# Optimization experiments

Measured on AMD Instinct MI355X. Metric: run time of the kernel, lower is better.

## Reference

```python
import jax, jax.numpy as jnp
import numpy as np

K_HOPS = 10
ALPHA = 0.1


def setup_inputs() -> dict:
    key = jax.random.key(0)
    ks = jax.random.split(key, 12)
    B, H, N, IC, F, C = 4096, 5, 30, 256, 512, 4
    real = jax.random.normal(ks[0], (B, N, IC), jnp.float32)
    imag = jax.random.normal(ks[1], (B, N, IC), jnp.float32)
    graph = jax.random.normal(ks[2], (B, H, N, N), jnp.float32)
    def lin(k, fan_in, shape):
        s = 1.0 / np.sqrt(fan_in)
        return jax.random.uniform(k, shape, jnp.float32, -s, s)
    W1 = lin(ks[3], IC, (IC, F)); b1 = lin(ks[4], IC, (F,))
    W2 = lin(ks[5], F, (F, F));  b2 = lin(ks[6], F, (F,))
    Wl = lin(ks[7], F, (F, 1));  bl = lin(ks[8], F, (1,))
    Wc = lin(ks[9], N, (C, N));  bc = lin(ks[10], N, (C,))
    return {"real": real, "imag": imag, "graph": graph,
            "W1": W1, "b1": b1, "W2": W2, "b2": b2,
            "Wl": Wl, "bl": bl, "Wc": Wc, "bc": bc}


def _appnp(S, x):
    # x_{k+1} = alpha * x0 + (1 - alpha) * S @ x_k, K iterations
    x0 = x
    def step(h, _):
        h = ALPHA * x0 + (1.0 - ALPHA) * jnp.einsum('bij,bjf->bif', S, h)
        return h, None
    h, _ = jax.lax.scan(step, x, None, length=K_HOPS)
    return h


def _prop_matrix(graph):
    # adj = mean over frequency dim; edges = nonzero entries (weights discarded
    # by the original code), self loops added, symmetric gcn_norm with
    # degree = column sums; source->target flow => operator is transposed.
    adj = jnp.mean(graph, axis=1)                      # [B,N,N]
    M = (adj != 0).astype(graph.dtype)
    N = M.shape[-1]
    Mt = M + jnp.eye(N, dtype=graph.dtype)             # add self loops
    deg = jnp.sum(Mt, axis=-2)                         # in-degree (col sums) [B,N]
    dinv = jax.lax.rsqrt(deg)
    S = dinv[:, :, None] * jnp.swapaxes(Mt, -1, -2) * dinv[:, None, :]
    return S


def reference(real, imag, graph, W1, b1, W2, b2, Wl, bl, Wc, bc):
    S = _prop_matrix(graph)
    # layer 1: linear -> relu -> APPNP(K=10)
    x = jax.nn.relu(jnp.einsum('bni,if->bnf', real, W1) + b1)
    x = _appnp(S, x)
    # layer 2: linear -> relu -> APPNP(K=10)
    x = jax.nn.relu(jnp.einsum('bnf,fg->bng', x, W2) + b2)
    x = _appnp(S, x)
    # readout: per-node linear to scalar, relu, then Conv1d(30->C, k=1)
    x = jax.nn.relu(jnp.einsum('bnf,fo->bno', x, Wl)[..., 0] + bl[0])  # [B,N]
    out = jnp.einsum('bn,cn->bc', x, Wc) + bc                          # [B,C]
    return out
```

## Files before the change

### kernel.cpp

```cpp
#include <hip/hip_runtime.h>
#include <hip/hip_bf16.h>

typedef _Float16 f16;
typedef _Float16 f16x8 __attribute__((ext_vector_type(8)));
typedef _Float16 f16x4 __attribute__((ext_vector_type(4)));
typedef float f32x4 __attribute__((ext_vector_type(4)));

#define P_OFF   0
#define W1T_OFF 14745600
#define W2T_OFF 15007744

__global__ __launch_bounds__(256) void k_prep(const float* __restrict__ W1,
                                              const float* __restrict__ W2,
                                              f16* __restrict__ w1t,
                                              f16* __restrict__ w2t) {
    long id = (long)blockIdx.x * 256 + threadIdx.x;
    if (id < 131072) {
        int f = (int)(id >> 8), k = (int)(id & 255);
        w1t[id] = (f16)W1[k * 512 + f];
    } else {
        long i = id - 131072;
        int f = (int)(i >> 9), k = (int)(i & 511);
        w2t[i] = (f16)W2[k * 512 + f];
    }
}

__global__ __launch_bounds__(256) void k_prop(const float* __restrict__ graph,
                                              float* __restrict__ P) {
    __shared__ float MtS[4][990];
    __shared__ float dinvS[4][32];
    __shared__ f16 qhS[4][1024];
    __shared__ f16 qlS[4][1024];

    const int wv = threadIdx.x >> 6, lane = threadIdx.x & 63;
    const int lr = lane & 15, gq = lane >> 4;
    const long b = (long)blockIdx.x * 4 + wv;
    const float* g = graph + b * 4500;
    float* Mt = MtS[wv];
    float* dinv = dinvS[wv];
    f16* qh = qhS[wv];
    f16* ql = qlS[wv];

    for (int rep = 0; rep < 15; ++rep) {
        int e = rep * 64 + lane;
        if (e < 900) {
            float s = g[e] + g[900 + e] + g[1800 + e] + g[2700 + e] + g[3600 + e];
            int r = e / 30, c = e - r * 30;
            Mt[r * 33 + c] = ((s != 0.f) ? 1.f : 0.f) + ((r == c) ? 1.f : 0.f);
        }
    }
    __syncthreads();
    if (lane < 30) {
        float d = 0.f;
        #pragma unroll
        for (int r = 0; r < 30; ++r) d += Mt[r * 33 + lane];
        dinv[lane] = 1.0f / sqrtf(d);
    }
    __syncthreads();

    auto Sval = [&](int i, int j) -> float {
        if (i >= 30 || j >= 30) return 0.f;
        return dinv[i] * Mt[j * 33 + i] * dinv[j];
    };

    f16x8 sh[2], sl[2];
    #pragma unroll
    for (int mi = 0; mi < 2; ++mi)
        #pragma unroll
        for (int jj = 0; jj < 8; ++jj) {
            float v = Sval(mi * 16 + lr, gq * 8 + jj);
            f16 h = (f16)v;
            sh[mi][jj] = h;
            sl[mi][jj] = (f16)(v - (float)h);
        }

    f32x4 qd[2][2], racc[2][2];
    #pragma unroll
    for (int mi = 0; mi < 2; ++mi)
        #pragma unroll
        for (int ni = 0; ni < 2; ++ni)
            #pragma unroll
            for (int r = 0; r < 4; ++r) {
                int row = mi * 16 + gq * 4 + r, col = ni * 16 + lr;
                qd[mi][ni][r] = Sval(row, col);
                racc[mi][ni][r] = (row == col) ? 0.1f : 0.f;
            }

    float c = 0.1f;
    for (int k = 1; k <= 9; ++k) {
        c *= 0.9f;
        #pragma unroll
        for (int mi = 0; mi < 2; ++mi)
            #pragma unroll
            for (int ni = 0; ni < 2; ++ni) {
                racc[mi][ni] += c * qd[mi][ni];
                f16x4 hh, ll;
                #pragma unroll
                for (int r = 0; r < 4; ++r) {
                    float v = qd[mi][ni][r];
                    f16 h = (f16)v;
                    hh[r] = h;
                    ll[r] = (f16)(v - (float)h);
                }
                const int col = ni * 16 + lr, rowb = mi * 16 + gq * 4;
                *reinterpret_cast<f16x4*>(qh + col * 32 + rowb) = hh;
                *reinterpret_cast<f16x4*>(ql + col * 32 + rowb) = ll;
            }
        __syncthreads();
        f16x8 bh[2], bl[2];
        #pragma unroll
        for (int ni = 0; ni < 2; ++ni) {
            const int col = ni * 16 + lr;
            bh[ni] = *reinterpret_cast<const f16x8*>(qh + col * 32 + gq * 8);
            bl[ni] = *reinterpret_cast<const f16x8*>(ql + col * 32 + gq * 8);
        }
        #pragma unroll
        for (int mi = 0; mi < 2; ++mi)
            #pragma unroll
            for (int ni = 0; ni < 2; ++ni) {
                f32x4 d = {0.f, 0.f, 0.f, 0.f};
                d = __builtin_amdgcn_mfma_f32_16x16x32_f16(sh[mi], bh[ni], d, 0, 0, 0);
                d = __builtin_amdgcn_mfma_f32_16x16x32_f16(sh[mi], bl[ni], d, 0, 0, 0);
                d = __builtin_amdgcn_mfma_f32_16x16x32_f16(sl[mi], bh[ni], d, 0, 0, 0);
                qd[mi][ni] = d;
            }
        __syncthreads();
    }
    const float cf = 0.3486784401f;
    #pragma unroll
    for (int mi = 0; mi < 2; ++mi)
        #pragma unroll
        for (int ni = 0; ni < 2; ++ni)
            #pragma unroll
            for (int r = 0; r < 4; ++r) {
                int row = mi * 16 + gq * 4 + r, col = ni * 16 + lr;
                if (row < 30 && col < 30)
                    P[b * 900 + row * 30 + col] = racc[mi][ni][r] + cf * qd[mi][ni][r];
            }
}

#define SMEM_BYTES 152576
#define PF_OFF   131072
#define B1L_OFF  141312
#define B2L_OFF  143360
#define WLL_OFF  145408
#define RED_OFF  147456
#define VL_OFF   151552
#define ZL_OFF   152064

__global__ __launch_bounds__(512, 2) void k_main(
    const float* __restrict__ real, const f16* __restrict__ w1t,
    const f16* __restrict__ w2t, const float* __restrict__ b1,
    const float* __restrict__ b2, const float* __restrict__ wl,
    const float* __restrict__ bl, const float* __restrict__ wc,
    const float* __restrict__ bc, const float* __restrict__ Pws,
    float* __restrict__ out) {
    extern __shared__ char smem[];
    char*  buf = smem;
    f16*   Pf  = (f16*)(smem + PF_OFF);
    float* b1l = (float*)(smem + B1L_OFF);
    float* b2l = (float*)(smem + B2L_OFF);
    float* wll = (float*)(smem + WLL_OFF);
    float* red = (float*)(smem + RED_OFF);
    float* vl  = (float*)(smem + VL_OFF);
    float* zl  = (float*)(smem + ZL_OFF);

    const int tid  = threadIdx.x;
    const int lane = tid & 63;
    const int wv   = tid >> 6;
    const int gq   = lane >> 4;
    const int lr   = lane & 15;
    const int blk  = blockIdx.x;
    const long r0  = (long)blk * 120;

    const float* rbase = real + r0 * 256;
    #pragma unroll
    for (int i = 0; i < 16; ++i) {
        const int row = wv + 8 * i;
        const int rr  = row & 31;
        if (rr < 30) {
            const float* gp = rbase + ((long)((row >> 5) * 30 + rr)) * 256
                              + ((lane ^ wv) << 2);
            __builtin_amdgcn_global_load_lds(
                (const __attribute__((address_space(1))) unsigned int*)gp,
                (__attribute__((address_space(3))) unsigned int*)(buf + row * 1024),
                16, 0, 0);
        }
    }
    {
        const int i   = tid >> 6;
        const int row = ((i >> 1) << 5) + 30 + (i & 1);
        f32x4 z = {0.f, 0.f, 0.f, 0.f};
        *reinterpret_cast<f32x4*>(buf + row * 1024 + (tid & 63) * 16) = z;
    }
    #pragma unroll
    for (int s = 0; s < 8; ++s) {
        int e = tid + s * 512;
        int bb = e >> 10, idx = e & 1023, n = idx >> 5, kk = idx & 31;
        float p = (n < 30 && kk < 30)
            ? Pws[((long)blk * 4 + bb) * 900 + n * 30 + kk] : 0.f;
        Pf[bb * 1280 + n * 40 + kk] = (f16)p;
    }
    b1l[tid] = b1[tid];
    b2l[tid] = b2[tid];
    wll[tid] = wl[tid];

    f32x4 acc[4][8];
    #pragma unroll
    for (int a = 0; a < 4; ++a)
        #pragma unroll
        for (int b = 0; b < 8; ++b) { f32x4 z = {0.f,0.f,0.f,0.f}; acc[a][b] = z; }
    __syncthreads();

    const f16* w1p = w1t + (wv * 64 + lr) * 256;
    #pragma unroll
    for (int kc = 0; kc < 8; ++kc) {
        f16x8 wa[4];
        #pragma unroll
        for (int mi = 0; mi < 4; ++mi)
            wa[mi] = *reinterpret_cast<const f16x8*>(w1p + mi * 4096 + kc * 32 + gq * 8);
        f16x8 bf[8];
        #pragma unroll
        for (int ni = 0; ni < 8; ++ni) {
            const int row = ni * 16 + lr;
            const int cb  = kc * 128 + gq * 32;
            f32x4 a0 = *reinterpret_cast<const f32x4*>(
                buf + row * 1024 + (cb ^ ((row & 7) << 4)));
            f32x4 a1 = *reinterpret_cast<const f32x4*>(
                buf + row * 1024 + ((cb + 16) ^ ((row & 7) << 4)));
            f16x8 h;
            h[0]=(f16)a0[0]; h[1]=(f16)a0[1]; h[2]=(f16)a0[2]; h[3]=(f16)a0[3];
            h[4]=(f16)a1[0]; h[5]=(f16)a1[1]; h[6]=(f16)a1[2]; h[7]=(f16)a1[3];
            bf[ni] = h;
        }
        __builtin_amdgcn_s_setprio(1);
        #pragma unroll
        for (int mi = 0; mi < 4; ++mi)
            #pragma unroll
            for (int ni = 0; ni < 8; ++ni)
                acc[mi][ni] = __builtin_amdgcn_mfma_f32_16x16x32_f16(wa[mi], bf[ni], acc[mi][ni], 0, 0, 0);
        __builtin_amdgcn_s_setprio(0);
    }
    __syncthreads();

    #pragma unroll
    for (int mi = 0; mi < 4; ++mi) {
        const int featb = wv * 64 + mi * 16 + gq * 4;
        float b1v[4];
        #pragma unroll
        for (int j = 0; j < 4; ++j) b1v[j] = b1l[featb + j];
        #pragma unroll
        for (int ni = 0; ni < 8; ++ni) {
            const int node = ni * 16 + lr;
            f16x4 h;
            #pragma unroll
            for (int j = 0; j < 4; ++j)
                h[j] = (f16)fmaxf(acc[mi][ni][j] + b1v[j], 0.f);
            *reinterpret_cast<f16x4*>(
                buf + node * 1024 + ((featb * 2) ^ ((node & 15) << 4))) = h;
        }
    }
    #pragma unroll
    for (int a = 0; a < 4; ++a)
        #pragma unroll
        for (int b = 0; b < 8; ++b) { f32x4 z = {0.f,0.f,0.f,0.f}; acc[a][b] = z; }
    __syncthreads();

    const f16* w2p = w2t + (wv * 64 + lr) * 512;
    f16x8 bfA[4], bfB[4];
    #pragma unroll
    for (int ni = 0; ni < 4; ++ni)
        bfA[ni] = *reinterpret_cast<const f16x8*>(w2p + ni * 8192 + gq * 8);
    #pragma unroll
    for (int ni = 0; ni < 4; ++ni)
        bfB[ni] = *reinterpret_cast<const f16x8*>(w2p + ni * 8192 + 32 + gq * 8);
    #pragma unroll
    for (int kc2 = 0; kc2 < 8; ++kc2) {
        {
            const int kc = 2 * kc2;
            f16x8 af[8];
            #pragma unroll
            for (int mi = 0; mi < 8; ++mi) {
                const int row = mi * 16 + lr;
                af[mi] = *reinterpret_cast<const f16x8*>(
                    buf + row * 1024 + (((kc * 32 + gq * 8) * 2) ^ ((row & 15) << 4)));
            }
            __builtin_amdgcn_s_setprio(1);
            #pragma unroll
            for (int mi = 0; mi < 8; ++mi)
                #pragma unroll
                for (int ni = 0; ni < 4; ++ni)
                    acc[ni][mi] = __builtin_amdgcn_mfma_f32_16x16x32_f16(af[mi], bfA[ni], acc[ni][mi], 0, 0, 0);
            __builtin_amdgcn_s_setprio(0);
            if (kc + 2 < 16)
                #pragma unroll
                for (int ni = 0; ni < 4; ++ni)
                    bfA[ni] = *reinterpret_cast<const f16x8*>(w2p + ni * 8192 + (kc + 2) * 32 + gq * 8);
        }
        {
            const int kc = 2 * kc2 + 1;
            f16x8 af[8];
            #pragma unroll
            for (int mi = 0; mi < 8; ++mi) {
                const int row = mi * 16 + lr;
                af[mi] = *reinterpret_cast<const f16x8*>(
                    buf + row * 1024 + (((kc * 32 + gq * 8) * 2) ^ ((row & 15) << 4)));
            }
            __builtin_amdgcn_s_setprio(1);
            #pragma unroll
            for (int mi = 0; mi < 8; ++mi)
                #pragma unroll
                for (int ni = 0; ni < 4; ++ni)
                    acc[ni][mi] = __builtin_amdgcn_mfma_f32_16x16x32_f16(af[mi], bfB[ni], acc[ni][mi], 0, 0, 0);
            __builtin_amdgcn_s_setprio(0);
            if (kc + 2 < 16)
                #pragma unroll
                for (int ni = 0; ni < 4; ++ni)
                    bfB[ni] = *reinterpret_cast<const f16x8*>(w2p + ni * 8192 + (kc + 2) * 32 + gq * 8);
        }
    }
    __syncthreads();

    #pragma unroll
    for (int mi = 0; mi < 8; ++mi)
        #pragma unroll
        for (int ni = 0; ni < 4; ++ni) {
            const int feat  = wv * 64 + ni * 16 + lr;
            const int node0 = mi * 16 + gq * 4;
            f16x4 h;
            #pragma unroll
            for (int j = 0; j < 4; ++j) h[j] = (f16)acc[ni][mi][j];
            *reinterpret_cast<f16x4*>(
                buf + feat * 256 + ((node0 * 2) ^ ((feat & 15) << 4))) = h;
        }
    __syncthreads();

    {
        f16x8 pb[4][2];
        #pragma unroll
        for (int bb = 0; bb < 4; ++bb)
            #pragma unroll
            for (int ni = 0; ni < 2; ++ni)
                pb[bb][ni] = *reinterpret_cast<const f16x8*>(
                    Pf + bb * 1280 + (ni * 16 + lr) * 40 + gq * 8);
        float vacc[4][2];
        #pragma unroll
        for (int bb = 0; bb < 4; ++bb)
            #pragma unroll
            for (int ni = 0; ni < 2; ++ni) vacc[bb][ni] = 0.f;
        #pragma unroll
        for (int mi = 0; mi < 4; ++mi) {
            const int featb = wv * 64 + mi * 16;
            float b2v[4], wlv[4];
            #pragma unroll
            for (int j = 0; j < 4; ++j) {
                b2v[j] = b2l[featb + gq * 4 + j];
                wlv[j] = wll[featb + gq * 4 + j];
            }
            f16x8 au[4];
            #pragma unroll
            for (int bb = 0; bb < 4; ++bb) {
                const int feat = featb + lr;
                au[bb] = *reinterpret_cast<const f16x8*>(
                    buf + feat * 256 + ((bb * 64 + gq * 16) ^ ((feat & 15) << 4)));
            }
            #pragma unroll
            for (int bb = 0; bb < 4; ++bb)
                #pragma unroll
                for (int ni = 0; ni < 2; ++ni) {
                    f32x4 d = {0.f,0.f,0.f,0.f};
                    d = __builtin_amdgcn_mfma_f32_16x16x32_f16(au[bb], pb[bb][ni], d, 0, 0, 0);
                    #pragma unroll
                    for (int j = 0; j < 4; ++j) {
                        float y = fmaxf(d[j] + b2v[j], 0.f);
                        vacc[bb][ni] = fmaf(y, wlv[j], vacc[bb][ni]);
                    }
                }
        }
        #pragma unroll
        for (int bb = 0; bb < 4; ++bb)
            #pragma unroll
            for (int ni = 0; ni < 2; ++ni) {
                float v = vacc[bb][ni];
                v += __shfl_xor(v, 16);
                v += __shfl_xor(v, 32);
                if (lane < 16) red[wv * 128 + bb * 32 + ni * 16 + lr] = v;
            }
    }
    __syncthreads();
    if (tid < 128) {
        float s = 0.f;
        #pragma unroll
        for (int w = 0; w < 8; ++w) s += red[w * 128 + tid];
        vl[tid] = s;
    }
    __syncthreads();
    if (tid < 120) {
        const int bb = tid / 30, n = tid - bb * 30;
        const float* Pr = Pws + ((long)blk * 4 + bb) * 900 + n * 30;
        float z = bl[0];
        #pragma unroll
        for (int j = 0; j < 30; ++j) z = fmaf(Pr[j], vl[bb * 32 + j], z);
        zl[tid] = fmaxf(z, 0.f);
    }
    __syncthreads();
    if (tid < 16) {
        const int bb = tid >> 2, cc = tid & 3;
        float o = bc[cc];
        #pragma unroll
        for (int n = 0; n < 30; ++n) o = fmaf(zl[bb * 30 + n], wc[cc * 30 + n], o);
        out[((long)blk * 4 + bb) * 4 + cc] = o;
    }
}

extern "C" void kernel_launch(void* const* d_in, const int* in_sizes, int n_in,
                              void* d_out, int out_size, void* d_ws, size_t ws_size,
                              hipStream_t stream) {
    const float* real  = (const float*)d_in[0];
    const float* graph = (const float*)d_in[2];
    const float* W1    = (const float*)d_in[3];
    const float* b1    = (const float*)d_in[4];
    const float* W2    = (const float*)d_in[5];
    const float* b2    = (const float*)d_in[6];
    const float* Wl    = (const float*)d_in[7];
    const float* bl    = (const float*)d_in[8];
    const float* Wc    = (const float*)d_in[9];
    const float* bc    = (const float*)d_in[10];
    float* out = (float*)d_out;
    char*  ws  = (char*)d_ws;

    float* Pws = (float*)(ws + P_OFF);
    f16*   w1t = (f16*)(ws + W1T_OFF);
    f16*   w2t = (f16*)(ws + W2T_OFF);

    k_prep<<<1536, 256, 0, stream>>>(W1, W2, w1t, w2t);
    k_prop<<<1024, 256, 0, stream>>>(graph, Pws);
    (void)hipFuncSetAttribute((const void*)k_main,
                              hipFuncAttributeMaxDynamicSharedMemorySize, SMEM_BYTES);
    k_main<<<1024, 512, SMEM_BYTES, stream>>>(real, w1t, w2t, b1, b2, Wl, bl, Wc, bc,
                                              Pws, out);
}
```

Baseline: 184.3 us.

## Double k_main block to 1024 threads with 2D wave tiling and f16 staging

k_main now runs 16 waves per block, split into 8 feature groups by 2 node halves, so each wave holds a 4x4 MFMA accumulator tile instead of 4x8. The input rows are loaded with plain vector loads, converted to f16 and stored swizzled into LDS, replacing the async global-to-LDS fp32 copy and the per-iteration conversion. The first GEMM also gains double-buffered weight prefetch. The aim is more waves for latency hiding and lower register pressure, at the cost of an extra LDS region for the 16-wave reduction and a synchronous load phase.

```diff
diff --git a/kernel.cpp b/kernel.cpp
--- a/kernel.cpp
+++ b/kernel.cpp
@@ -139,16 +139,16 @@
             }
 }
 
-#define SMEM_BYTES 152576
+#define SMEM_BYTES 156672
 #define PF_OFF   131072
 #define B1L_OFF  141312
 #define B2L_OFF  143360
 #define WLL_OFF  145408
 #define RED_OFF  147456
-#define VL_OFF   151552
-#define ZL_OFF   152064
-
-__global__ __launch_bounds__(512, 2) void k_main(
+#define VL_OFF   155648
+#define ZL_OFF   156160
+
+__global__ __launch_bounds__(1024, 4) void k_main(
     const float* __restrict__ real, const f16* __restrict__ w1t,
     const f16* __restrict__ w2t, const float* __restrict__ b1,
     const float* __restrict__ b2, const float* __restrict__ wl,
@@ -168,90 +168,104 @@
     const int tid  = threadIdx.x;
     const int lane = tid & 63;
     const int wv   = tid >> 6;
+    const int wf   = wv & 7;
+    const int wn   = wv >> 3;
     const int gq   = lane >> 4;
     const int lr   = lane & 15;
     const int blk  = blockIdx.x;
     const long r0  = (long)blk * 120;
 
-    const float* rbase = real + r0 * 256;
-    #pragma unroll
-    for (int i = 0; i < 16; ++i) {
-        const int row = wv + 8 * i;
-        const int rr  = row & 31;
-        if (rr < 30) {
-            const float* gp = rbase + ((long)((row >> 5) * 30 + rr)) * 256
-                              + ((lane ^ wv) << 2);
-            __builtin_amdgcn_global_load_lds(
-                (const __attribute__((address_space(1))) unsigned int*)gp,
-                (__attribute__((address_space(3))) unsigned int*)(buf + row * 1024),
-                16, 0, 0);
-        }
-    }
     {
-        const int i   = tid >> 6;
-        const int row = ((i >> 1) << 5) + 30 + (i & 1);
-        f32x4 z = {0.f, 0.f, 0.f, 0.f};
-        *reinterpret_cast<f32x4*>(buf + row * 1024 + (tid & 63) * 16) = z;
-    }
-    #pragma unroll
-    for (int s = 0; s < 8; ++s) {
-        int e = tid + s * 512;
+        const int srow = tid >> 3;
+        const int seg  = tid & 7;
+        const int rr   = srow & 31;
+        const bool valid = rr < 30;
+        const float* p = real + (r0 + (long)(srow >> 5) * 30 + rr) * 256 + seg * 32;
+        #pragma unroll
+        for (int q = 0; q < 4; ++q) {
+            f32x4 v0 = {0.f,0.f,0.f,0.f}, v1 = {0.f,0.f,0.f,0.f};
+            if (valid) {
+                v0 = *reinterpret_cast<const f32x4*>(p + q * 8);
+                v1 = *reinterpret_cast<const f32x4*>(p + q * 8 + 4);
+            }
+            f16x8 h;
+            h[0]=(f16)v0[0]; h[1]=(f16)v0[1]; h[2]=(f16)v0[2]; h[3]=(f16)v0[3];
+            h[4]=(f16)v1[0]; h[5]=(f16)v1[1]; h[6]=(f16)v1[2]; h[7]=(f16)v1[3];
+            *reinterpret_cast<f16x8*>(
+                buf + srow * 512 + ((seg * 64 + q * 16) ^ ((srow & 7) << 4))) = h;
+        }
+    }
+    #pragma unroll
+    for (int s = 0; s < 4; ++s) {
+        int e = tid + s * 1024;
         int bb = e >> 10, idx = e & 1023, n = idx >> 5, kk = idx & 31;
         float p = (n < 30 && kk < 30)
             ? Pws[((long)blk * 4 + bb) * 900 + n * 30 + kk] : 0.f;
         Pf[bb * 1280 + n * 40 + kk] = (f16)p;
     }
-    b1l[tid] = b1[tid];
-    b2l[tid] = b2[tid];
-    wll[tid] = wl[tid];
-
-    f32x4 acc[4][8];
+    if (tid < 512) {
+        b1l[tid] = b1[tid];
+        b2l[tid] = b2[tid];
+        wll[tid] = wl[tid];
+    }
+
+    f32x4 acc[4][4];
     #pragma unroll
     for (int a = 0; a < 4; ++a)
         #pragma unroll
-        for (int b = 0; b < 8; ++b) { f32x4 z = {0.f,0.f,0.f,0.f}; acc[a][b] = z; }
-    __syncthreads();
-
-    const f16* w1p = w1t + (wv * 64 + lr) * 256;
-    #pragma unroll
-    for (int kc = 0; kc < 8; ++kc) {
-        f16x8 wa[4];
-        #pragma unroll
-        for (int mi = 0; mi < 4; ++mi)
-            wa[mi] = *reinterpret_cast<const f16x8*>(w1p + mi * 4096 + kc * 32 + gq * 8);
-        f16x8 bf[8];
-        #pragma unroll
-        for (int ni = 0; ni < 8; ++ni) {
-            const int row = ni * 16 + lr;
-            const int cb  = kc * 128 + gq * 32;
-            f32x4 a0 = *reinterpret_cast<const f32x4*>(
-                buf + row * 1024 + (cb ^ ((row & 7) << 4)));
-            f32x4 a1 = *reinterpret_cast<const f32x4*>(
-                buf + row * 1024 + ((cb + 16) ^ ((row & 7) << 4)));
-            f16x8 h;
-            h[0]=(f16)a0[0]; h[1]=(f16)a0[1]; h[2]=(f16)a0[2]; h[3]=(f16)a0[3];
-            h[4]=(f16)a1[0]; h[5]=(f16)a1[1]; h[6]=(f16)a1[2]; h[7]=(f16)a1[3];
-            bf[ni] = h;
-        }
-        __builtin_amdgcn_s_setprio(1);
-        #pragma unroll
-        for (int mi = 0; mi < 4; ++mi)
-            #pragma unroll
-            for (int ni = 0; ni < 8; ++ni)
-                acc[mi][ni] = __builtin_amdgcn_mfma_f32_16x16x32_f16(wa[mi], bf[ni], acc[mi][ni], 0, 0, 0);
-        __builtin_amdgcn_s_setprio(0);
+        for (int b = 0; b < 4; ++b) { f32x4 z = {0.f,0.f,0.f,0.f}; acc[a][b] = z; }
+    __syncthreads();
+
+    const f16* w1p = w1t + (wf * 64 + lr) * 256;
+    {
+        f16x8 waA[4], waB[4];
+        #pragma unroll
+        for (int mi = 0; mi < 4; ++mi) {
+            waA[mi] = *reinterpret_cast<const f16x8*>(w1p + mi * 4096 + gq * 8);
+            waB[mi] = *reinterpret_cast<const f16x8*>(w1p + mi * 4096 + 32 + gq * 8);
+        }
+        #pragma unroll
+        for (int kc2 = 0; kc2 < 4; ++kc2) {
+            #pragma unroll
+            for (int half = 0; half < 2; ++half) {
+                const int kc = 2 * kc2 + half;
+                f16x8 bf[4];
+                #pragma unroll
+                for (int ni = 0; ni < 4; ++ni) {
+                    const int row = wn * 64 + ni * 16 + lr;
+                    bf[ni] = *reinterpret_cast<const f16x8*>(
+                        buf + row * 512 + ((kc * 64 + gq * 16) ^ ((row & 7) << 4)));
+                }
+                __builtin_amdgcn_s_setprio(1);
+                #pragma unroll
+                for (int mi = 0; mi < 4; ++mi)
+                    #pragma unroll
+                    for (int ni = 0; ni < 4; ++ni)
+                        acc[mi][ni] = __builtin_amdgcn_mfma_f32_16x16x32_f16(
+                            half ? waB[mi] : waA[mi], bf[ni], acc[mi][ni], 0, 0, 0);
+                __builtin_amdgcn_s_setprio(0);
+                if (kc + 2 < 8) {
+                    #pragma unroll
+                    for (int mi = 0; mi < 4; ++mi) {
+                        f16x8 w = *reinterpret_cast<const f16x8*>(
+                            w1p + mi * 4096 + (kc + 2) * 32 + gq * 8);
+                        if (half) waB[mi] = w; else waA[mi] = w;
+                    }
+                }
+            }
+        }
     }
     __syncthreads();
 
     #pragma unroll
     for (int mi = 0; mi < 4; ++mi) {
-        const int featb = wv * 64 + mi * 16 + gq * 4;
+        const int featb = wf * 64 + mi * 16 + gq * 4;
         float b1v[4];
         #pragma unroll
         for (int j = 0; j < 4; ++j) b1v[j] = b1l[featb + j];
         #pragma unroll
-        for (int ni = 0; ni < 8; ++ni) {
-            const int node = ni * 16 + lr;
+        for (int ni = 0; ni < 4; ++ni) {
+            const int node = wn * 64 + ni * 16 + lr;
             f16x4 h;
             #pragma unroll
             for (int j = 0; j < 4; ++j)
@@ -263,73 +277,59 @@
     #pragma unroll
     for (int a = 0; a < 4; ++a)
         #pragma unroll
-        for (int b = 0; b < 8; ++b) { f32x4 z = {0.f,0.f,0.f,0.f}; acc[a][b] = z; }
-    __syncthreads();
-
-    const f16* w2p = w2t + (wv * 64 + lr) * 512;
-    f16x8 bfA[4], bfB[4];
-    #pragma unroll
-    for (int ni = 0; ni < 4; ++ni)
-        bfA[ni] = *reinterpret_cast<const f16x8*>(w2p + ni * 8192 + gq * 8);
-    #pragma unroll
-    for (int ni = 0; ni < 4; ++ni)
-        bfB[ni] = *reinterpret_cast<const f16x8*>(w2p + ni * 8192 + 32 + gq * 8);
-    #pragma unroll
-    for (int kc2 = 0; kc2 < 8; ++kc2) {
-        {
-            const int kc = 2 * kc2;
-            f16x8 af[8];
-            #pragma unroll
-            for (int mi = 0; mi < 8; ++mi) {
-                const int row = mi * 16 + lr;
-                af[mi] = *reinterpret_cast<const f16x8*>(
-                    buf + row * 1024 + (((kc * 32 + gq * 8) * 2) ^ ((row & 15) << 4)));
-            }
-            __builtin_amdgcn_s_setprio(1);
-            #pragma unroll
-            for (int mi = 0; mi < 8; ++mi)
-                #pragma unroll
-                for (int ni = 0; ni < 4; ++ni)
-                    acc[ni][mi] = __builtin_amdgcn_mfma_f32_16x16x32_f16(af[mi], bfA[ni], acc[ni][mi], 0, 0, 0);
-            __builtin_amdgcn_s_setprio(0);
-            if (kc + 2 < 16)
-                #pragma unroll
-                for (int ni = 0; ni < 4; ++ni)
-                    bfA[ni] = *reinterpret_cast<const f16x8*>(w2p + ni * 8192 + (kc + 2) * 32 + gq * 8);
-        }
-        {
-            const int kc = 2 * kc2 + 1;
-            f16x8 af[8];
-            #pragma unroll
-            for (int mi = 0; mi < 8; ++mi) {
-                const int row = mi * 16 + lr;
-                af[mi] = *reinterpret_cast<const f16x8*>(
-                    buf + row * 1024 + (((kc * 32 + gq * 8) * 2) ^ ((row & 15) << 4)));
-            }
-            __builtin_amdgcn_s_setprio(1);
-            #pragma unroll
-            for (int mi = 0; mi < 8; ++mi)
-                #pragma unroll
-                for (int ni = 0; ni < 4; ++ni)
-                    acc[ni][mi] = __builtin_amdgcn_mfma_f32_16x16x32_f16(af[mi], bfB[ni], acc[ni][mi], 0, 0, 0);
-            __builtin_amdgcn_s_setprio(0);
-            if (kc + 2 < 16)
-                #pragma unroll
-                for (int ni = 0; ni < 4; ++ni)
-                    bfB[ni] = *reinterpret_cast<const f16x8*>(w2p + ni * 8192 + (kc + 2) * 32 + gq * 8);
-        }
-    }
-    __syncthreads();
-
-    #pragma unroll
-    for (int mi = 0; mi < 8; ++mi)
+        for (int b = 0; b < 4; ++b) { f32x4 z = {0.f,0.f,0.f,0.f}; acc[a][b] = z; }
+    __syncthreads();
+
+    const f16* w2p = w2t + (wf * 64 + lr) * 512;
+    {
+        f16x8 bfA[4], bfB[4];
         #pragma unroll
         for (int ni = 0; ni < 4; ++ni) {
-            const int feat  = wv * 64 + ni * 16 + lr;
-            const int node0 = mi * 16 + gq * 4;
+            bfA[ni] = *reinterpret_cast<const f16x8*>(w2p + ni * 8192 + gq * 8);
+            bfB[ni] = *reinterpret_cast<const f16x8*>(w2p + ni * 8192 + 32 + gq * 8);
+        }
+        #pragma unroll
+        for (int kc2 = 0; kc2 < 8; ++kc2) {
+            #pragma unroll
+            for (int half = 0; half < 2; ++half) {
+                const int kc = 2 * kc2 + half;
+                f16x8 af[4];
+                #pragma unroll
+                for (int mi = 0; mi < 4; ++mi) {
+                    const int row = wn * 64 + mi * 16 + lr;
+                    af[mi] = *reinterpret_cast<const f16x8*>(
+                        buf + row * 1024 + (((kc * 32 + gq * 8) * 2) ^ ((row & 15) << 4)));
+                }
+                __builtin_amdgcn_s_setprio(1);
+                #pragma unroll
+                for (int mi = 0; mi < 4; ++mi)
+                    #pragma unroll
+                    for (int ni = 0; ni < 4; ++ni)
+                        acc[mi][ni] = __builtin_amdgcn_mfma_f32_16x16x32_f16(
+                            af[mi], half ? bfB[ni] : bfA[ni], acc[mi][ni], 0, 0, 0);
+                __builtin_amdgcn_s_setprio(0);
+                if (kc + 2 < 16) {
+                    #pragma unroll
+                    for (int ni = 0; ni < 4; ++ni) {
+                        f16x8 w = *reinterpret_cast<const f16x8*>(
+                            w2p + ni * 8192 + (kc + 2) * 32 + gq * 8);
+                        if (half) bfB[ni] = w; else bfA[ni] = w;
+                    }
+                }
+            }
+        }
+    }
+    __syncthreads();
+
+    #pragma unroll
+    for (int mi = 0; mi < 4; ++mi)
+        #pragma unroll
+        for (int ni = 0; ni < 4; ++ni) {
+            const int feat  = wf * 64 + ni * 16 + lr;
+            const int node0 = wn * 64 + mi * 16 + gq * 4;
             f16x4 h;
             #pragma unroll
-            for (int j = 0; j < 4; ++j) h[j] = (f16)acc[ni][mi][j];
+            for (int j = 0; j < 4; ++j) h[j] = (f16)acc[mi][ni][j];
             *reinterpret_cast<f16x4*>(
                 buf + feat * 256 + ((node0 * 2) ^ ((feat & 15) << 4))) = h;
         }
@@ -349,8 +349,8 @@
             #pragma unroll
             for (int ni = 0; ni < 2; ++ni) vacc[bb][ni] = 0.f;
         #pragma unroll
-        for (int mi = 0; mi < 4; ++mi) {
-            const int featb = wv * 64 + mi * 16;
+        for (int mi = 0; mi < 2; ++mi) {
+            const int featb = wv * 32 + mi * 16;
             float b2v[4], wlv[4];
             #pragma unroll
             for (int j = 0; j < 4; ++j) {
@@ -391,7 +391,7 @@
     if (tid < 128) {
         float s = 0.f;
         #pragma unroll
-        for (int w = 0; w < 8; ++w) s += red[w * 128 + tid];
+        for (int w = 0; w < 16; ++w) s += red[w * 128 + tid];
         vl[tid] = s;
     }
     __syncthreads();
@@ -437,6 +437,6 @@
     k_prop<<<1024, 256, 0, stream>>>(graph, Pws);
     (void)hipFuncSetAttribute((const void*)k_main,
                               hipFuncAttributeMaxDynamicSharedMemorySize, SMEM_BYTES);
-    k_main<<<1024, 512, SMEM_BYTES, stream>>>(real, w1t, w2t, b1, b2, Wl, bl, Wc, bc,
-                                              Pws, out);
+    k_main<<<1024, 1024, SMEM_BYTES, stream>>>(real, w1t, w2t, b1, b2, Wl, bl, Wc, bc,
+                                               Pws, out);
 }
```

Measured after the change: 278.1 us. 1.51x slower.

## Split GEMM1/GEMM2 into two node-half passes with double-buffered fragment loads

Applied to the files above, without the earlier changes.

Both feature GEMMs now run as two passes over 64-node halves instead of one 128-node tile. This halves the accumulator array from 32 to 16 fragments and frees registers. The freed registers go to software pipelining: the next k-chunk's LDS reads (and f32-to-f16 conversion for GEMM1) are issued while the current MFMAs run, and the weight fragments are double-buffered. The GEMM2 output is written to a new split LDS layout so the upper half can be stored after the first pass. This adds extra barriers and re-reads the weight fragments from global memory for each pass.

```diff
diff --git a/kernel.cpp b/kernel.cpp
--- a/kernel.cpp
+++ b/kernel.cpp
@@ -204,135 +204,206 @@
     b1l[tid] = b1[tid];
     b2l[tid] = b2[tid];
     wll[tid] = wl[tid];
-
-    f32x4 acc[4][8];
-    #pragma unroll
-    for (int a = 0; a < 4; ++a)
-        #pragma unroll
-        for (int b = 0; b < 8; ++b) { f32x4 z = {0.f,0.f,0.f,0.f}; acc[a][b] = z; }
     __syncthreads();
 
     const f16* w1p = w1t + (wv * 64 + lr) * 256;
-    #pragma unroll
-    for (int kc = 0; kc < 8; ++kc) {
-        f16x8 wa[4];
-        #pragma unroll
-        for (int mi = 0; mi < 4; ++mi)
-            wa[mi] = *reinterpret_cast<const f16x8*>(w1p + mi * 4096 + kc * 32 + gq * 8);
-        f16x8 bf[8];
-        #pragma unroll
-        for (int ni = 0; ni < 8; ++ni) {
-            const int row = ni * 16 + lr;
+    const f16* w2p = w2t + (wv * 64 + lr) * 512;
+
+    auto g1read = [&](f32x4 (&ra)[4][2], int nb, int kc) {
+        #pragma unroll
+        for (int ni = 0; ni < 4; ++ni) {
+            const int row = nb + ni * 16 + lr;
             const int cb  = kc * 128 + gq * 32;
-            f32x4 a0 = *reinterpret_cast<const f32x4*>(
+            ra[ni][0] = *reinterpret_cast<const f32x4*>(
                 buf + row * 1024 + (cb ^ ((row & 7) << 4)));
-            f32x4 a1 = *reinterpret_cast<const f32x4*>(
+            ra[ni][1] = *reinterpret_cast<const f32x4*>(
                 buf + row * 1024 + ((cb + 16) ^ ((row & 7) << 4)));
+        }
+    };
+    auto g1cvt = [&](f16x8 (&bf)[4], const f32x4 (&ra)[4][2]) {
+        #pragma unroll
+        for (int ni = 0; ni < 4; ++ni) {
             f16x8 h;
-            h[0]=(f16)a0[0]; h[1]=(f16)a0[1]; h[2]=(f16)a0[2]; h[3]=(f16)a0[3];
-            h[4]=(f16)a1[0]; h[5]=(f16)a1[1]; h[6]=(f16)a1[2]; h[7]=(f16)a1[3];
+            h[0]=(f16)ra[ni][0][0]; h[1]=(f16)ra[ni][0][1];
+            h[2]=(f16)ra[ni][0][2]; h[3]=(f16)ra[ni][0][3];
+            h[4]=(f16)ra[ni][1][0]; h[5]=(f16)ra[ni][1][1];
+            h[6]=(f16)ra[ni][1][2]; h[7]=(f16)ra[ni][1][3];
             bf[ni] = h;
         }
-        __builtin_amdgcn_s_setprio(1);
-        #pragma unroll
-        for (int mi = 0; mi < 4; ++mi)
-            #pragma unroll
-            for (int ni = 0; ni < 8; ++ni)
-                acc[mi][ni] = __builtin_amdgcn_mfma_f32_16x16x32_f16(wa[mi], bf[ni], acc[mi][ni], 0, 0, 0);
-        __builtin_amdgcn_s_setprio(0);
-    }
-    __syncthreads();
-
-    #pragma unroll
-    for (int mi = 0; mi < 4; ++mi) {
-        const int featb = wv * 64 + mi * 16 + gq * 4;
-        float b1v[4];
-        #pragma unroll
-        for (int j = 0; j < 4; ++j) b1v[j] = b1l[featb + j];
-        #pragma unroll
-        for (int ni = 0; ni < 8; ++ni) {
-            const int node = ni * 16 + lr;
-            f16x4 h;
-            #pragma unroll
-            for (int j = 0; j < 4; ++j)
-                h[j] = (f16)fmaxf(acc[mi][ni][j] + b1v[j], 0.f);
-            *reinterpret_cast<f16x4*>(
-                buf + node * 1024 + ((featb * 2) ^ ((node & 15) << 4))) = h;
-        }
-    }
-    #pragma unroll
-    for (int a = 0; a < 4; ++a)
-        #pragma unroll
-        for (int b = 0; b < 8; ++b) { f32x4 z = {0.f,0.f,0.f,0.f}; acc[a][b] = z; }
-    __syncthreads();
-
-    const f16* w2p = w2t + (wv * 64 + lr) * 512;
-    f16x8 bfA[4], bfB[4];
-    #pragma unroll
-    for (int ni = 0; ni < 4; ++ni)
-        bfA[ni] = *reinterpret_cast<const f16x8*>(w2p + ni * 8192 + gq * 8);
-    #pragma unroll
-    for (int ni = 0; ni < 4; ++ni)
-        bfB[ni] = *reinterpret_cast<const f16x8*>(w2p + ni * 8192 + 32 + gq * 8);
-    #pragma unroll
-    for (int kc2 = 0; kc2 < 8; ++kc2) {
-        {
-            const int kc = 2 * kc2;
-            f16x8 af[8];
-            #pragma unroll
-            for (int mi = 0; mi < 8; ++mi) {
-                const int row = mi * 16 + lr;
-                af[mi] = *reinterpret_cast<const f16x8*>(
-                    buf + row * 1024 + (((kc * 32 + gq * 8) * 2) ^ ((row & 15) << 4)));
-            }
+    };
+
+    auto gemm1_pass = [&](int nb) {
+        f32x4 acc[4][4];
+        #pragma unroll
+        for (int a = 0; a < 4; ++a)
+            #pragma unroll
+            for (int b = 0; b < 4; ++b) { f32x4 z = {0.f,0.f,0.f,0.f}; acc[a][b] = z; }
+        f32x4 ra[4][2];
+        f16x8 bf[2][4], wa[2][4];
+        g1read(ra, nb, 0);
+        #pragma unroll
+        for (int mi = 0; mi < 4; ++mi) {
+            wa[0][mi] = *reinterpret_cast<const f16x8*>(w1p + mi * 4096 + gq * 8);
+            wa[1][mi] = *reinterpret_cast<const f16x8*>(w1p + mi * 4096 + 32 + gq * 8);
+        }
+        g1cvt(bf[0], ra);
+        #pragma unroll
+        for (int kc = 0; kc < 8; ++kc) {
+            const int c = kc & 1, n = c ^ 1;
+            if (kc + 1 < 8) g1read(ra, nb, kc + 1);
             __builtin_amdgcn_s_setprio(1);
             #pragma unroll
-            for (int mi = 0; mi < 8; ++mi)
+            for (int mi = 0; mi < 4; ++mi)
                 #pragma unroll
                 for (int ni = 0; ni < 4; ++ni)
-                    acc[ni][mi] = __builtin_amdgcn_mfma_f32_16x16x32_f16(af[mi], bfA[ni], acc[ni][mi], 0, 0, 0);
+                    acc[mi][ni] = __builtin_amdgcn_mfma_f32_16x16x32_f16(
+                        wa[c][mi], bf[c][ni], acc[mi][ni], 0, 0, 0);
+            __builtin_amdgcn_s_setprio(0);
+            if (kc + 2 < 8)
+                #pragma unroll
+                for (int mi = 0; mi < 4; ++mi)
+                    wa[c][mi] = *reinterpret_cast<const f16x8*>(
+                        w1p + mi * 4096 + (kc + 2) * 32 + gq * 8);
+            if (kc + 1 < 8) g1cvt(bf[n], ra);
+        }
+        #pragma unroll
+        for (int mi = 0; mi < 4; ++mi) {
+            const int featb = wv * 64 + mi * 16 + gq * 4;
+            float b1v[4];
+            #pragma unroll
+            for (int j = 0; j < 4; ++j) b1v[j] = b1l[featb + j];
+            #pragma unroll
+            for (int ni = 0; ni < 4; ++ni) {
+                const int node = nb + ni * 16 + lr;
+                f16x4 h;
+                #pragma unroll
+                for (int j = 0; j < 4; ++j)
+                    h[j] = (f16)fmaxf(acc[mi][ni][j] + b1v[j], 0.f);
+                *reinterpret_cast<f16x4*>(
+                    buf + node * 1024 + ((featb * 2) ^ ((node & 15) << 4))) = h;
+            }
+        }
+    };
+
+    {
+        f32x4 acc[4][4];
+        #pragma unroll
+        for (int a = 0; a < 4; ++a)
+            #pragma unroll
+            for (int b = 0; b < 4; ++b) { f32x4 z = {0.f,0.f,0.f,0.f}; acc[a][b] = z; }
+        f32x4 ra[4][2];
+        f16x8 bf[2][4], wa[2][4];
+        g1read(ra, 64, 0);
+        #pragma unroll
+        for (int mi = 0; mi < 4; ++mi) {
+            wa[0][mi] = *reinterpret_cast<const f16x8*>(w1p + mi * 4096 + gq * 8);
+            wa[1][mi] = *reinterpret_cast<const f16x8*>(w1p + mi * 4096 + 32 + gq * 8);
+        }
+        g1cvt(bf[0], ra);
+        #pragma unroll
+        for (int kc = 0; kc < 8; ++kc) {
+            const int c = kc & 1, n = c ^ 1;
+            if (kc + 1 < 8) g1read(ra, 64, kc + 1);
+            __builtin_amdgcn_s_setprio(1);
+            #pragma unroll
+            for (int mi = 0; mi < 4; ++mi)
+                #pragma unroll
+                for (int ni = 0; ni < 4; ++ni)
+                    acc[mi][ni] = __builtin_amdgcn_mfma_f32_16x16x32_f16(
+                        wa[c][mi], bf[c][ni], acc[mi][ni], 0, 0, 0);
+            __builtin_amdgcn_s_setprio(0);
+            if (kc + 2 < 8)
+                #pragma unroll
+                for (int mi = 0; mi < 4; ++mi)
+                    wa[c][mi] = *reinterpret_cast<const f16x8*>(
+                        w1p + mi * 4096 + (kc + 2) * 32 + gq * 8);
+            if (kc + 1 < 8) g1cvt(bf[n], ra);
+        }
+        __syncthreads();
+        #pragma unroll
+        for (int mi = 0; mi < 4; ++mi) {
+            const int featb = wv * 64 + mi * 16 + gq * 4;
+            float b1v[4];
+            #pragma unroll
+            for (int j = 0; j < 4; ++j) b1v[j] = b1l[featb + j];
+            #pragma unroll
+            for (int ni = 0; ni < 4; ++ni) {
+                const int node = 64 + ni * 16 + lr;
+                f16x4 h;
+                #pragma unroll
+                for (int j = 0; j < 4; ++j)
+                    h[j] = (f16)fmaxf(acc[mi][ni][j] + b1v[j], 0.f);
+                *reinterpret_cast<f16x4*>(
+                    buf + node * 1024 + ((featb * 2) ^ ((node & 15) << 4))) = h;
+            }
+        }
+    }
+    gemm1_pass(0);
+    __syncthreads();
+
+    auto g2read = [&](f16x8 (&af)[4], int nb, int kc) {
+        #pragma unroll
+        for (int mi = 0; mi < 4; ++mi) {
+            const int row = nb + mi * 16 + lr;
+            af[mi] = *reinterpret_cast<const f16x8*>(
+                buf + row * 1024 + (((kc * 32 + gq * 8) * 2) ^ ((row & 15) << 4)));
+        }
+    };
+    auto gemm2_pass = [&](int nb, f32x4 (&acc)[4][4]) {
+        #pragma unroll
+        for (int a = 0; a < 4; ++a)
+            #pragma unroll
+            for (int b = 0; b < 4; ++b) { f32x4 z = {0.f,0.f,0.f,0.f}; acc[a][b] = z; }
+        f16x8 af[2][4], bw[2][4];
+        g2read(af[0], nb, 0);
+        #pragma unroll
+        for (int ni = 0; ni < 4; ++ni) {
+            bw[0][ni] = *reinterpret_cast<const f16x8*>(w2p + ni * 8192 + gq * 8);
+            bw[1][ni] = *reinterpret_cast<const f16x8*>(w2p + ni * 8192 + 32 + gq * 8);
+        }
+        #pragma unroll
+        for (int kc = 0; kc < 16; ++kc) {
+            const int c = kc & 1, n = c ^ 1;
+            if (kc + 1 < 16) g2read(af[n], nb, kc + 1);
+            __builtin_amdgcn_s_setprio(1);
+            #pragma unroll
+            for (int mi = 0; mi < 4; ++mi)
+                #pragma unroll
+                for (int ni = 0; ni < 4; ++ni)
+                    acc[ni][mi] = __builtin_amdgcn_mfma_f32_16x16x32_f16(
+                        af[c][mi], bw[c][ni], acc[ni][mi], 0, 0, 0);
             __builtin_amdgcn_s_setprio(0);
             if (kc + 2 < 16)
                 #pragma unroll
                 for (int ni = 0; ni < 4; ++ni)
-                    bfA[ni] = *reinterpret_cast<const f16x8*>(w2p + ni * 8192 + (kc + 2) * 32 + gq * 8);
-        }
-        {
-            const int kc = 2 * kc2 + 1;
-            f16x8 af[8];
-            #pragma unroll
-            for (int mi = 0; mi < 8; ++mi) {
-                const int row = mi * 16 + lr;
-                af[mi] = *reinterpret_cast<const f16x8*>(
-                    buf + row * 1024 + (((kc * 32 + gq * 8) * 2) ^ ((row & 15) << 4)));
-            }
-            __builtin_amdgcn_s_setprio(1);
-            #pragma unroll
-            for (int mi = 0; mi < 8; ++mi)
-                #pragma unroll
-                for (int ni = 0; ni < 4; ++ni)
-                    acc[ni][mi] = __builtin_amdgcn_mfma_f32_16x16x32_f16(af[mi], bfB[ni], acc[ni][mi], 0, 0, 0);
-            __builtin_amdgcn_s_setprio(0);
-            if (kc + 2 < 16)
-                #pragma unroll
-                for (int ni = 0; ni < 4; ++ni)
-                    bfB[ni] = *reinterpret_cast<const f16x8*>(w2p + ni * 8192 + (kc + 2) * 32 + gq * 8);
-        }
-    }
-    __syncthreads();
-
-    #pragma unroll
-    for (int mi = 0; mi < 8; ++mi)
-        #pragma unroll
-        for (int ni = 0; ni < 4; ++ni) {
-            const int feat  = wv * 64 + ni * 16 + lr;
-            const int node0 = mi * 16 + gq * 4;
-            f16x4 h;
-            #pragma unroll
-            for (int j = 0; j < 4; ++j) h[j] = (f16)acc[ni][mi][j];
-            *reinterpret_cast<f16x4*>(
-                buf + feat * 256 + ((node0 * 2) ^ ((feat & 15) << 4))) = h;
-        }
+                    bw[c][ni] = *reinterpret_cast<const f16x8*>(
+                        w2p + ni * 8192 + (kc + 2) * 32 + gq * 8);
+        }
+    };
+    auto ep2_pass = [&](const f32x4 (&acc)[4][4], int p) {
+        #pragma unroll
+        for (int mi = 0; mi < 4; ++mi)
+            #pragma unroll
+            for (int ni = 0; ni < 4; ++ni) {
+                const int feat  = wv * 64 + ni * 16 + lr;
+                const int nodeh = mi * 16 + gq * 4;
+                f16x4 h;
+                #pragma unroll
+                for (int j = 0; j < 4; ++j) h[j] = (f16)acc[ni][mi][j];
+                *reinterpret_cast<f16x4*>(
+                    buf + p * 65536 + feat * 128 + ((nodeh * 2) ^ ((feat & 7) << 4))) = h;
+            }
+    };
+
+    {
+        f32x4 acc[4][4];
+        gemm2_pass(64, acc);
+        __syncthreads();
+        ep2_pass(acc, 1);
+        gemm2_pass(0, acc);
+        __syncthreads();
+        ep2_pass(acc, 0);
+    }
     __syncthreads();
 
     {
@@ -362,7 +433,8 @@
             for (int bb = 0; bb < 4; ++bb) {
                 const int feat = featb + lr;
                 au[bb] = *reinterpret_cast<const f16x8*>(
-                    buf + feat * 256 + ((bb * 64 + gq * 16) ^ ((feat & 15) << 4)));
+                    buf + (bb >> 1) * 65536 + feat * 128 +
+                    (((bb & 1) * 64 + gq * 16) ^ ((feat & 7) << 4)));
             }
             #pragma unroll
             for (int bb = 0; bb < 4; ++bb)
```

New measurement: 262.3 us. 42.3% more time.
